# Kernel optimization log

Hardware: AMD Instinct MI355X
Metric: run time of the kernel (lower is better)

The kernel has to match this reference:

```python
import jax, jax.numpy as jnp
import numpy as np

NUM_CLASSES = 3
SMOOTH = 1e-5
EPS = 1e-6
ITERS = 8
W_CL = 0.5


def maxpool3d(x):
    # 3x3x3 max pool, stride 1, padding 1 (pads with -inf, matching torch max_pool3d)
    return jax.lax.reduce_window(
        x, -jnp.inf, jax.lax.max,
        window_dimensions=(1, 1, 3, 3, 3),
        window_strides=(1, 1, 1, 1, 1),
        padding=[(0, 0), (0, 0), (1, 1), (1, 1), (1, 1)])


def soft_skeletonize_3d(x, iters=ITERS):
    for _ in range(iters):
        eroded = 1.0 - maxpool3d(1.0 - x)
        opened = maxpool3d(eroded)
        contour = jax.nn.relu(opened - eroded)
        x = jax.nn.relu(x - contour)
    return x


def setup_inputs() -> dict:
    key = jax.random.key(0)
    k1, k2 = jax.random.split(key)
    logits = jax.random.normal(k1, (2, 3, 160, 160, 160), dtype=jnp.float32)
    target = jax.random.randint(k2, (2, 160, 160, 160), 0, NUM_CLASSES, dtype=jnp.int64)
    return {"logits": logits, "target": target}


def reference(logits, target):
    # ---- DiceCE ----
    logp = jax.nn.log_softmax(logits, axis=1)                      # [B,C,D,H,W]
    ce = -jnp.mean(jnp.take_along_axis(logp, target[:, None], axis=1))
    probs = jnp.exp(logp)
    onehot = jax.lax.stop_gradient(
        jax.nn.one_hot(target, NUM_CLASSES, axis=1, dtype=probs.dtype))
    dims = (0, 2, 3, 4)
    intersect = jnp.sum(probs * onehot, axis=dims)                 # [C]
    pred_sum = jnp.sum(probs, axis=dims)
    targ_sum = jnp.sum(onehot, axis=dims)
    dice_per_class = (2.0 * intersect + SMOOTH) / (pred_sum + targ_sum + SMOOTH)
    base = ce + (1.0 - jnp.mean(dice_per_class))
    # ---- soft clDice ----
    p_v = jnp.clip(1.0 - probs[:, :1], 0.0, 1.0)                   # [B,1,D,H,W]
    y_v = 1.0 - onehot[:, :1]
    p_skel = soft_skeletonize_3d(p_v)
    y_skel = soft_skeletonize_3d(y_v)
    tprec = jnp.sum(p_skel * y_v) / (jnp.sum(p_skel) + EPS)
    tsens = jnp.sum(y_skel * p_v) / (jnp.sum(y_skel) + EPS)
    cldice = 2.0 * tprec * tsens / (tprec + tsens + EPS)
    return base + W_CL * (1.0 - cldice)
```

## Files before the change

kernel.cpp:

```cpp
#include <hip/hip_runtime.h>
#include <math.h>

#define B_    2
#define DDIM  160
#define HDIM  160
#define WDIM  160
#define DHW   (DDIM*HDIM*WDIM)
#define NVOX  (B_*DHW)
#define NGRP  (NVOX/4)
#define ITERS 8
#define DT    4

#define SMOOTHF 1e-5
#define EPSF    1e-6
#define W_CL    0.5

#define NB1 2048
#define NQ1 10
#define NB2 2048
#define NQ2 4

#define NROWS (B_*DDIM*HDIM)
#define YW    8
#define NYW   (NROWS*YW)

#define P_THREADS (10*HDIM*(DDIM/DT)*B_)
#define P_BLOCKS  (P_THREADS/256)
#define Y_BLOCKS  (NROWS/256)
#define F_BLOCKS  (P_BLOCKS + Y_BLOCKS)

#define OFF_P1 0
#define OFF_P2 (NB1*NQ1*8)
#define HEADER_BYTES 262144


__device__ inline double wave_reduce(double v) {
    #pragma unroll
    for (int off = 32; off > 0; off >>= 1)
        v += __shfl_down(v, off, 64);
    return v;
}

template<int NQ>
__device__ inline void block_reduce_store(double* vals, double* out) {
    __shared__ double smem[NQ][4];
    int lane = threadIdx.x & 63;
    int wid  = threadIdx.x >> 6;
    #pragma unroll
    for (int q = 0; q < NQ; ++q) {
        double v = wave_reduce(vals[q]);
        if (lane == 0) smem[q][wid] = v;
    }
    __syncthreads();
    if (threadIdx.x == 0) {
        #pragma unroll
        for (int q = 0; q < NQ; ++q)
            out[q] = smem[q][0] + smem[q][1] + smem[q][2] + smem[q][3];
    }
}


__global__ void init_kernel(const float* __restrict__ logits,
                            const int*   __restrict__ target,
                            float* __restrict__ porig,
                            double* __restrict__ partials)
{
    double acc[NQ1];
    #pragma unroll
    for (int q = 0; q < NQ1; ++q) acc[q] = 0.0;

    int tid = blockIdx.x * blockDim.x + threadIdx.x;
    int stride = gridDim.x * blockDim.x;
    for (int g = tid; g < NGRP; g += stride) {
        int i = g * 4;
        int b = i / DHW;
        int s = i - b * DHW;
        const float* base = logits + (size_t)b * (3 * DHW) + s;
        float4 l0 = *(const float4*)(base);
        float4 l1 = *(const float4*)(base + DHW);
        float4 l2 = *(const float4*)(base + 2 * DHW);
        int4 tg = *(const int4*)(target + i);

        float pv[4];
        const float* a0 = (const float*)&l0;
        const float* a1 = (const float*)&l1;
        const float* a2 = (const float*)&l2;
        const int*   tt = (const int*)&tg;
        #pragma unroll
        for (int j = 0; j < 4; ++j) {
            float x0 = a0[j], x1 = a1[j], x2 = a2[j];
            float m  = fmaxf(x0, fmaxf(x1, x2));
            float e0 = __expf(x0 - m), e1 = __expf(x1 - m), e2 = __expf(x2 - m);
            float sum = e0 + e1 + e2;
            float inv = 1.0f / sum;
            float q0 = e0 * inv, q1 = e1 * inv, q2 = e2 * inv;
            int t = tt[j];
            float lt = (t == 0) ? x0 : ((t == 1) ? x1 : x2);
            float logp_t = (lt - m) - __logf(sum);
            acc[0] += (double)(-logp_t);
            acc[4] += (double)q0; acc[5] += (double)q1; acc[6] += (double)q2;
            if (t == 0)      { acc[1] += (double)q0; acc[7] += 1.0; }
            else if (t == 1) { acc[2] += (double)q1; acc[8] += 1.0; }
            else             { acc[3] += (double)q2; acc[9] += 1.0; }
            float p = 1.0f - q0;
            pv[j] = fminf(fmaxf(p, 0.0f), 1.0f);
        }
        *(float4*)(porig + i) = make_float4(pv[0], pv[1], pv[2], pv[3]);
    }
    block_reduce_store<NQ1>(acc, partials + (size_t)blockIdx.x * NQ1);
}


__global__ void ybits_init(const int* __restrict__ target,
                           unsigned* __restrict__ yb)
{
    int tid = blockIdx.x * 256 + threadIdx.x;
    int k = tid % YW;
    int rowlin = tid / YW;
    unsigned word = 0u;
    if (k < 5) {
        const int* t = target + (size_t)rowlin * WDIM + k * 32;
        #pragma unroll
        for (int q = 0; q < 8; ++q) {
            int4 v = *(const int4*)(t + q * 4);
            if (v.x) word |= 1u << (q * 4 + 0);
            if (v.y) word |= 1u << (q * 4 + 1);
            if (v.z) word |= 1u << (q * 4 + 2);
            if (v.w) word |= 1u << (q * 4 + 3);
        }
    }
    yb[tid] = word;
}


__device__ inline void row18(const float* __restrict__ row, int w0, float pad, float* e) {
    float4 f;
    f = *(const float4*)(row + 0);  e[1]=f.x;  e[2]=f.y;  e[3]=f.z;  e[4]=f.w;
    f = *(const float4*)(row + 4);  e[5]=f.x;  e[6]=f.y;  e[7]=f.z;  e[8]=f.w;
    f = *(const float4*)(row + 8);  e[9]=f.x;  e[10]=f.y; e[11]=f.z; e[12]=f.w;
    f = *(const float4*)(row + 12); e[13]=f.x; e[14]=f.y; e[15]=f.z; e[16]=f.w;
    e[0]  = (w0 > 0)         ? row[-1] : pad;
    e[17] = (w0 + 16 < WDIM) ? row[16] : pad;
}

__device__ inline void load_yrow(const unsigned* __restrict__ base, unsigned* r) {
    uint4 v = *(const uint4*)base;
    r[0] = v.x; r[1] = v.y; r[2] = v.z; r[3] = v.w; r[4] = base[4];
}

__device__ inline void werode_row(const unsigned* r, unsigned* out) {
    #pragma unroll
    for (int k = 0; k < 5; ++k) {
        unsigned l  = (r[k] << 1) | (k > 0 ? (r[k-1] >> 31) : 1u);
        unsigned rt = (r[k] >> 1) | (k < 4 ? (r[k+1] << 31) : 0x80000000u);
        out[k] = r[k] & l & rt;
    }
}

__device__ inline void wdilate_row(const unsigned* r, unsigned* out) {
    #pragma unroll
    for (int k = 0; k < 5; ++k) {
        unsigned l  = (r[k] << 1) | (k > 0 ? (r[k-1] >> 31) : 0u);
        unsigned rt = (r[k] >> 1) | (k < 4 ? (r[k+1] << 31) : 0u);
        out[k] = r[k] | l | rt;
    }
}


__global__ void fused_erode(const float* __restrict__ x, float* __restrict__ er,
                            const unsigned* __restrict__ yb, unsigned* __restrict__ eb)
{
    if (blockIdx.x < P_BLOCKS) {
        int tid = blockIdx.x * 256 + threadIdx.x;
        int w16 = tid % 10;
        int t2  = tid / 10;
        int h   = t2 % HDIM;
        int t3  = t2 / HDIM;
        int dc  = t3 % (DDIM / DT);
        int vol = t3 / (DDIM / DT);
        int w0  = w16 * 16;
        int d0  = dc * DT;
        const float* src = x + (size_t)vol * DHW;
        float*       dst = er + (size_t)vol * DHW;

        float ring[3][16];
        #pragma unroll
        for (int step = 0; step < DT + 2; ++step) {
            int d = d0 - 1 + step;
            float cur[16];
            #pragma unroll
            for (int i = 0; i < 16; ++i) cur[i] = INFINITY;
            if ((unsigned)d < (unsigned)DDIM) {
                #pragma unroll
                for (int dy = -1; dy <= 1; ++dy) {
                    int y = h + dy;
                    if ((unsigned)y >= (unsigned)HDIM) continue;
                    const float* row = src + ((size_t)d * HDIM + y) * WDIM + w0;
                    float e[18];
                    row18(row, w0, INFINITY, e);
                    #pragma unroll
                    for (int i = 0; i < 16; ++i)
                        cur[i] = fminf(cur[i], fminf(e[i], fminf(e[i+1], e[i+2])));
                }
            }
            #pragma unroll
            for (int i = 0; i < 16; ++i) ring[step % 3][i] = cur[i];
            if (step >= 2) {
                int dd = d - 1;
                float* o = dst + ((size_t)dd * HDIM + h) * WDIM + w0;
                #pragma unroll
                for (int q = 0; q < 4; ++q) {
                    float4 v;
                    v.x = fminf(ring[0][q*4+0], fminf(ring[1][q*4+0], ring[2][q*4+0]));
                    v.y = fminf(ring[0][q*4+1], fminf(ring[1][q*4+1], ring[2][q*4+1]));
                    v.z = fminf(ring[0][q*4+2], fminf(ring[1][q*4+2], ring[2][q*4+2]));
                    v.w = fminf(ring[0][q*4+3], fminf(ring[1][q*4+3], ring[2][q*4+3]));
                    *(float4*)(o + q*4) = v;
                }
            }
        }
    } else {
        int tid = (blockIdx.x - P_BLOCKS) * 256 + threadIdx.x;
        int h  = tid % HDIM;
        int t2 = tid / HDIM;
        int d  = t2 % DDIM;
        int b  = t2 / DDIM;
        unsigned acc[5] = {~0u, ~0u, ~0u, ~0u, ~0u};
        #pragma unroll
        for (int dz = -1; dz <= 1; ++dz) {
            int z = d + dz; if ((unsigned)z >= (unsigned)DDIM) continue;
            #pragma unroll
            for (int dy = -1; dy <= 1; ++dy) {
                int y = h + dy; if ((unsigned)y >= (unsigned)HDIM) continue;
                unsigned r[5], we[5];
                load_yrow(yb + ((size_t)(b * DDIM + z) * HDIM + y) * YW, r);
                werode_row(r, we);
                #pragma unroll
                for (int k = 0; k < 5; ++k) acc[k] &= we[k];
            }
        }
        unsigned* o = eb + (size_t)tid * YW;
        *(uint4*)o = make_uint4(acc[0], acc[1], acc[2], acc[3]);
        o[4] = acc[4];
    }
}


__global__ void fused_open(const float* __restrict__ er,
                           const float* __restrict__ xsrc, float* __restrict__ xdst,
                           const unsigned* __restrict__ eb, unsigned* __restrict__ yb)
{
    if (blockIdx.x < P_BLOCKS) {
        int tid = blockIdx.x * 256 + threadIdx.x;
        int w16 = tid % 10;
        int t2  = tid / 10;
        int h   = t2 % HDIM;
        int t3  = t2 / HDIM;
        int dc  = t3 % (DDIM / DT);
        int vol = t3 / (DDIM / DT);
        int w0  = w16 * 16;
        int d0  = dc * DT;
        const float* ers = er + (size_t)vol * DHW;
        const float* xs  = xsrc + (size_t)vol * DHW;
        float*       xb  = xdst + (size_t)vol * DHW;

        float ring[3][16];
        #pragma unroll
        for (int step = 0; step < DT + 2; ++step) {
            int d = d0 - 1 + step;
            float cur[16];
            #pragma unroll
            for (int i = 0; i < 16; ++i) cur[i] = -INFINITY;
            if ((unsigned)d < (unsigned)DDIM) {
                #pragma unroll
                for (int dy = -1; dy <= 1; ++dy) {
                    int y = h + dy;
                    if ((unsigned)y >= (unsigned)HDIM) continue;
                    const float* row = ers + ((size_t)d * HDIM + y) * WDIM + w0;
                    float e[18];
                    row18(row, w0, -INFINITY, e);
                    #pragma unroll
                    for (int i = 0; i < 16; ++i)
                        cur[i] = fmaxf(cur[i], fmaxf(e[i], fmaxf(e[i+1], e[i+2])));
                }
            }
            #pragma unroll
            for (int i = 0; i < 16; ++i) ring[step % 3][i] = cur[i];
            if (step >= 2) {
                int dd = d - 1;
                size_t idx = ((size_t)dd * HDIM + h) * WDIM + w0;
                #pragma unroll
                for (int q = 0; q < 4; ++q) {
                    float4 ec = *(const float4*)(ers + idx + q*4);
                    float4 xv = *(const float4*)(xs + idx + q*4);
                    float o0 = fmaxf(ring[0][q*4+0], fmaxf(ring[1][q*4+0], ring[2][q*4+0]));
                    float o1 = fmaxf(ring[0][q*4+1], fmaxf(ring[1][q*4+1], ring[2][q*4+1]));
                    float o2 = fmaxf(ring[0][q*4+2], fmaxf(ring[1][q*4+2], ring[2][q*4+2]));
                    float o3 = fmaxf(ring[0][q*4+3], fmaxf(ring[1][q*4+3], ring[2][q*4+3]));
                    float4 r;
                    r.x = fmaxf(xv.x - fmaxf(o0 - ec.x, 0.0f), 0.0f);
                    r.y = fmaxf(xv.y - fmaxf(o1 - ec.y, 0.0f), 0.0f);
                    r.z = fmaxf(xv.z - fmaxf(o2 - ec.z, 0.0f), 0.0f);
                    r.w = fmaxf(xv.w - fmaxf(o3 - ec.w, 0.0f), 0.0f);
                    *(float4*)(xb + idx + q*4) = r;
                }
            }
        }
    } else {
        int tid = (blockIdx.x - P_BLOCKS) * 256 + threadIdx.x;
        int h  = tid % HDIM;
        int t2 = tid / HDIM;
        int d  = t2 % DDIM;
        int b  = t2 / DDIM;
        unsigned acc[5] = {0u, 0u, 0u, 0u, 0u};
        unsigned ecen[5];
        #pragma unroll
        for (int dz = -1; dz <= 1; ++dz) {
            int z = d + dz; if ((unsigned)z >= (unsigned)DDIM) continue;
            #pragma unroll
            for (int dy = -1; dy <= 1; ++dy) {
                int y = h + dy; if ((unsigned)y >= (unsigned)HDIM) continue;
                unsigned r[5], wd[5];
                load_yrow(eb + ((size_t)(b * DDIM + z) * HDIM + y) * YW, r);
                if (dz == 0 && dy == 0) {
                    #pragma unroll
                    for (int k = 0; k < 5; ++k) ecen[k] = r[k];
                }
                wdilate_row(r, wd);
                #pragma unroll
                for (int k = 0; k < 5; ++k) acc[k] |= wd[k];
            }
        }
        unsigned* yo = yb + (size_t)tid * YW;
        unsigned yr[5];
        load_yrow(yo, yr);
        unsigned out[5];
        #pragma unroll
        for (int k = 0; k < 5; ++k)
            out[k] = yr[k] & ~(acc[k] & ~ecen[k]);
        *(uint4*)yo = make_uint4(out[0], out[1], out[2], out[3]);
        yo[4] = out[4];
    }
}


__global__ void final_reduce_kernel(const float* __restrict__ porig,
                                    const float* __restrict__ pskel,
                                    const int*   __restrict__ target,
                                    const unsigned* __restrict__ yb,
                                    double* __restrict__ partials)
{
    double acc[NQ2];
    #pragma unroll
    for (int q = 0; q < NQ2; ++q) acc[q] = 0.0;

    int tid = blockIdx.x * blockDim.x + threadIdx.x;
    int stride = gridDim.x * blockDim.x;
    for (int g = tid; g < NGRP; g += stride) {
        int i = g * 4;
        float4 ps = *(const float4*)(pskel + i);
        float4 po = *(const float4*)(porig + i);
        int4   tg = *(const int4*)(target + i);
        int w = i % WDIM;
        int rowlin = i / WDIM;
        unsigned word = yb[(size_t)rowlin * YW + (w >> 5)];
        unsigned b4 = (word >> (w & 31)) & 0xFu;
        const float* psp = (const float*)&ps;
        const float* pop = (const float*)&po;
        const int*   tp  = (const int*)&tg;
        #pragma unroll
        for (int j = 0; j < 4; ++j) {
            float yv  = (tp[j] != 0) ? 1.0f : 0.0f;
            float ysk = (float)((b4 >> j) & 1u);
            acc[0] += (double)(psp[j] * yv);
            acc[1] += (double)psp[j];
            acc[2] += (double)(ysk * pop[j]);
            acc[3] += (double)ysk;
        }
    }
    block_reduce_store<NQ2>(acc, partials + (size_t)blockIdx.x * NQ2);
}


__global__ void finalize_kernel(const double* __restrict__ p1,
                                const double* __restrict__ p2,
                                float* __restrict__ out)
{
    double acc[NQ1 + NQ2];
    #pragma unroll
    for (int q = 0; q < NQ1 + NQ2; ++q) acc[q] = 0.0;

    for (int b = threadIdx.x; b < NB1; b += 256) {
        #pragma unroll
        for (int q = 0; q < NQ1; ++q) acc[q] += p1[(size_t)b * NQ1 + q];
    }
    for (int b = threadIdx.x; b < NB2; b += 256) {
        #pragma unroll
        for (int q = 0; q < NQ2; ++q) acc[NQ1 + q] += p2[(size_t)b * NQ2 + q];
    }

    __shared__ double smem[NQ1 + NQ2][4];
    int lane = threadIdx.x & 63;
    int wid  = threadIdx.x >> 6;
    #pragma unroll
    for (int q = 0; q < NQ1 + NQ2; ++q) {
        double v = wave_reduce(acc[q]);
        if (lane == 0) smem[q][wid] = v;
    }
    __syncthreads();
    if (threadIdx.x == 0) {
        double a[NQ1 + NQ2];
        #pragma unroll
        for (int q = 0; q < NQ1 + NQ2; ++q)
            a[q] = smem[q][0] + smem[q][1] + smem[q][2] + smem[q][3];

        double ce = a[0] / (double)NVOX;
        double dice = 0.0;
        #pragma unroll
        for (int c = 0; c < 3; ++c) {
            double I = a[1 + c], P = a[4 + c], T = a[7 + c];
            dice += (2.0 * I + SMOOTHF) / (P + T + SMOOTHF);
        }
        dice *= (1.0 / 3.0);
        double base = ce + (1.0 - dice);

        double tprec = a[10] / (a[11] + EPSF);
        double tsens = a[12] / (a[13] + EPSF);
        double cld = 2.0 * tprec * tsens / (tprec + tsens + EPSF);
        out[0] = (float)(base + W_CL * (1.0 - cld));
    }
}


extern "C" void kernel_launch(void* const* d_in, const int* in_sizes, int n_in,
                              void* d_out, int out_size, void* d_ws, size_t ws_size,
                              hipStream_t stream) {
    const float* logits = (const float*)d_in[0];
    const int*   target = (const int*)d_in[1];

    double* partials1 = (double*)((char*)d_ws + OFF_P1);
    double* partials2 = (double*)((char*)d_ws + OFF_P2);
    float*  porig = (float*)((char*)d_ws + HEADER_BYTES);
    float*  pskel = porig + NVOX;
    float*  er    = pskel + NVOX;
    unsigned* ybits  = (unsigned*)(er + NVOX);
    unsigned* yebits = ybits + NYW;

    init_kernel<<<NB1, 256, 0, stream>>>(logits, target, porig, partials1);
    ybits_init<<<NYW / 256, 256, 0, stream>>>(target, ybits);

    for (int it = 0; it < ITERS; ++it) {
        const float* xsrc = (it == 0) ? porig : pskel;
        fused_erode<<<F_BLOCKS, 256, 0, stream>>>(xsrc, er, ybits, yebits);
        fused_open<<<F_BLOCKS, 256, 0, stream>>>(er, xsrc, pskel, yebits, ybits);
    }

    final_reduce_kernel<<<NB2, 256, 0, stream>>>(porig, pskel, target, ybits, partials2);
    finalize_kernel<<<1, 256, 0, stream>>>(partials1, partials2, (float*)d_out);
}
```

Measured before the change: 656.3 us.

## Store skeleton field in fp16 and do min/max on raw half bits

```diff
diff --git a/kernel.cpp b/kernel.cpp
--- a/kernel.cpp
+++ b/kernel.cpp
@@ -1,4 +1,5 @@
 #include <hip/hip_runtime.h>
+#include <hip/hip_fp16.h>
 #include <math.h>
 
 #define B_    2
@@ -29,9 +30,25 @@
 #define Y_BLOCKS  (NROWS/256)
 #define F_BLOCKS  (P_BLOCKS + Y_BLOCKS)
 
+#define PAD_MIN 0x7C00u
+#define PAD_MAX 0x0000u
+
 #define OFF_P1 0
 #define OFF_P2 (NB1*NQ1*8)
 #define HEADER_BYTES 262144
+
+typedef unsigned short u16;
+
+
+__device__ inline u16 umn(u16 a, u16 b) { return a < b ? a : b; }
+__device__ inline u16 umx(u16 a, u16 b) { return a > b ? a : b; }
+
+__device__ inline float us2f(u16 u) {
+    __half h; __builtin_memcpy(&h, &u, 2); return __half2float(h);
+}
+__device__ inline u16 f2us(float f) {
+    __half h = __float2half(f); u16 u; __builtin_memcpy(&u, &h, 2); return u;
+}
 
 
 __device__ inline double wave_reduce(double v) {
@@ -63,11 +80,12 @@
 __global__ void init_kernel(const float* __restrict__ logits,
                             const int*   __restrict__ target,
                             float* __restrict__ porig,
+                            u16*   __restrict__ p16,
                             double* __restrict__ partials)
 {
-    double acc[NQ1];
-    #pragma unroll
-    for (int q = 0; q < NQ1; ++q) acc[q] = 0.0;
+    float facc[NQ1];
+    #pragma unroll
+    for (int q = 0; q < NQ1; ++q) facc[q] = 0.0f;
 
     int tid = blockIdx.x * blockDim.x + threadIdx.x;
     int stride = gridDim.x * blockDim.x;
@@ -97,16 +115,23 @@
             int t = tt[j];
             float lt = (t == 0) ? x0 : ((t == 1) ? x1 : x2);
             float logp_t = (lt - m) - __logf(sum);
-            acc[0] += (double)(-logp_t);
-            acc[4] += (double)q0; acc[5] += (double)q1; acc[6] += (double)q2;
-            if (t == 0)      { acc[1] += (double)q0; acc[7] += 1.0; }
-            else if (t == 1) { acc[2] += (double)q1; acc[8] += 1.0; }
-            else             { acc[3] += (double)q2; acc[9] += 1.0; }
+            facc[0] += -logp_t;
+            facc[4] += q0; facc[5] += q1; facc[6] += q2;
+            if (t == 0)      { facc[1] += q0; facc[7] += 1.0f; }
+            else if (t == 1) { facc[2] += q1; facc[8] += 1.0f; }
+            else             { facc[3] += q2; facc[9] += 1.0f; }
             float p = 1.0f - q0;
             pv[j] = fminf(fmaxf(p, 0.0f), 1.0f);
         }
         *(float4*)(porig + i) = make_float4(pv[0], pv[1], pv[2], pv[3]);
-    }
+        union { uint2 v; u16 u[4]; } ph;
+        #pragma unroll
+        for (int j = 0; j < 4; ++j) ph.u[j] = f2us(pv[j]);
+        *(uint2*)(p16 + i) = ph.v;
+    }
+    double acc[NQ1];
+    #pragma unroll
+    for (int q = 0; q < NQ1; ++q) acc[q] = (double)facc[q];
     block_reduce_store<NQ1>(acc, partials + (size_t)blockIdx.x * NQ1);
 }
 
@@ -133,14 +158,22 @@
 }
 
 
-__device__ inline void row18(const float* __restrict__ row, int w0, float pad, float* e) {
-    float4 f;
-    f = *(const float4*)(row + 0);  e[1]=f.x;  e[2]=f.y;  e[3]=f.z;  e[4]=f.w;
-    f = *(const float4*)(row + 4);  e[5]=f.x;  e[6]=f.y;  e[7]=f.z;  e[8]=f.w;
-    f = *(const float4*)(row + 8);  e[9]=f.x;  e[10]=f.y; e[11]=f.z; e[12]=f.w;
-    f = *(const float4*)(row + 12); e[13]=f.x; e[14]=f.y; e[15]=f.z; e[16]=f.w;
+__device__ inline void rowload_h(const u16* __restrict__ row, int w0, u16 pad, u16* e) {
+    union { uint4 v; u16 u[8]; } a, b;
+    a.v = *(const uint4*)(row);
+    b.v = *(const uint4*)(row + 8);
+    #pragma unroll
+    for (int i = 0; i < 8; ++i) { e[1 + i] = a.u[i]; e[9 + i] = b.u[i]; }
     e[0]  = (w0 > 0)         ? row[-1] : pad;
     e[17] = (w0 + 16 < WDIM) ? row[16] : pad;
+}
+
+__device__ inline void store16_h(u16* __restrict__ o, const u16* v) {
+    union { uint4 q; u16 u[8]; } s0, s1;
+    #pragma unroll
+    for (int i = 0; i < 8; ++i) { s0.u[i] = v[i]; s1.u[i] = v[8 + i]; }
+    *(uint4*)(o)     = s0.q;
+    *(uint4*)(o + 8) = s1.q;
 }
 
 __device__ inline void load_yrow(const unsigned* __restrict__ base, unsigned* r) {
@@ -167,7 +200,7 @@
 }
 
 
-__global__ void fused_erode(const float* __restrict__ x, float* __restrict__ er,
+__global__ void fused_erode(const u16* __restrict__ x, u16* __restrict__ er,
                             const unsigned* __restrict__ yb, unsigned* __restrict__ eb)
 {
     if (blockIdx.x < P_BLOCKS) {
@@ -180,43 +213,38 @@
         int vol = t3 / (DDIM / DT);
         int w0  = w16 * 16;
         int d0  = dc * DT;
-        const float* src = x + (size_t)vol * DHW;
-        float*       dst = er + (size_t)vol * DHW;
-
-        float ring[3][16];
+        const u16* src = x + (size_t)vol * DHW;
+        u16*       dst = er + (size_t)vol * DHW;
+
+        u16 ring[3][16];
         #pragma unroll
         for (int step = 0; step < DT + 2; ++step) {
             int d = d0 - 1 + step;
-            float cur[16];
-            #pragma unroll
-            for (int i = 0; i < 16; ++i) cur[i] = INFINITY;
+            u16 cur[16];
+            #pragma unroll
+            for (int i = 0; i < 16; ++i) cur[i] = PAD_MIN;
             if ((unsigned)d < (unsigned)DDIM) {
                 #pragma unroll
                 for (int dy = -1; dy <= 1; ++dy) {
                     int y = h + dy;
                     if ((unsigned)y >= (unsigned)HDIM) continue;
-                    const float* row = src + ((size_t)d * HDIM + y) * WDIM + w0;
-                    float e[18];
-                    row18(row, w0, INFINITY, e);
+                    const u16* row = src + ((size_t)d * HDIM + y) * WDIM + w0;
+                    u16 e[18];
+                    rowload_h(row, w0, PAD_MIN, e);
                     #pragma unroll
                     for (int i = 0; i < 16; ++i)
-                        cur[i] = fminf(cur[i], fminf(e[i], fminf(e[i+1], e[i+2])));
+                        cur[i] = umn(cur[i], umn(e[i], umn(e[i+1], e[i+2])));
                 }
             }
             #pragma unroll
             for (int i = 0; i < 16; ++i) ring[step % 3][i] = cur[i];
             if (step >= 2) {
                 int dd = d - 1;
-                float* o = dst + ((size_t)dd * HDIM + h) * WDIM + w0;
-                #pragma unroll
-                for (int q = 0; q < 4; ++q) {
-                    float4 v;
-                    v.x = fminf(ring[0][q*4+0], fminf(ring[1][q*4+0], ring[2][q*4+0]));
-                    v.y = fminf(ring[0][q*4+1], fminf(ring[1][q*4+1], ring[2][q*4+1]));
-                    v.z = fminf(ring[0][q*4+2], fminf(ring[1][q*4+2], ring[2][q*4+2]));
-                    v.w = fminf(ring[0][q*4+3], fminf(ring[1][q*4+3], ring[2][q*4+3]));
-                    *(float4*)(o + q*4) = v;
-                }
+                u16 out[16];
+                #pragma unroll
+                for (int i = 0; i < 16; ++i)
+                    out[i] = umn(ring[0][i], umn(ring[1][i], ring[2][i]));
+                store16_h(dst + ((size_t)dd * HDIM + h) * WDIM + w0, out);
             }
         }
     } else {
@@ -246,8 +274,8 @@
 }
 
 
-__global__ void fused_open(const float* __restrict__ er,
-                           const float* __restrict__ xsrc, float* __restrict__ xdst,
+__global__ void fused_open(const u16* __restrict__ er,
+                           const u16* __restrict__ xsrc, u16* __restrict__ xdst,
                            const unsigned* __restrict__ eb, unsigned* __restrict__ yb)
 {
     if (blockIdx.x < P_BLOCKS) {
@@ -260,28 +288,28 @@
         int vol = t3 / (DDIM / DT);
         int w0  = w16 * 16;
         int d0  = dc * DT;
-        const float* ers = er + (size_t)vol * DHW;
-        const float* xs  = xsrc + (size_t)vol * DHW;
-        float*       xb  = xdst + (size_t)vol * DHW;
-
-        float ring[3][16];
+        const u16* ers = er + (size_t)vol * DHW;
+        const u16* xs  = xsrc + (size_t)vol * DHW;
+        u16*       xb  = xdst + (size_t)vol * DHW;
+
+        u16 ring[3][16];
         #pragma unroll
         for (int step = 0; step < DT + 2; ++step) {
             int d = d0 - 1 + step;
-            float cur[16];
-            #pragma unroll
-            for (int i = 0; i < 16; ++i) cur[i] = -INFINITY;
+            u16 cur[16];
+            #pragma unroll
+            for (int i = 0; i < 16; ++i) cur[i] = PAD_MAX;
             if ((unsigned)d < (unsigned)DDIM) {
                 #pragma unroll
                 for (int dy = -1; dy <= 1; ++dy) {
                     int y = h + dy;
                     if ((unsigned)y >= (unsigned)HDIM) continue;
-                    const float* row = ers + ((size_t)d * HDIM + y) * WDIM + w0;
-                    float e[18];
-                    row18(row, w0, -INFINITY, e);
+                    const u16* row = ers + ((size_t)d * HDIM + y) * WDIM + w0;
+                    u16 e[18];
+                    rowload_h(row, w0, PAD_MAX, e);
                     #pragma unroll
                     for (int i = 0; i < 16; ++i)
-                        cur[i] = fmaxf(cur[i], fmaxf(e[i], fmaxf(e[i+1], e[i+2])));
+                        cur[i] = umx(cur[i], umx(e[i], umx(e[i+1], e[i+2])));
                 }
             }
             #pragma unroll
@@ -289,21 +317,20 @@
             if (step >= 2) {
                 int dd = d - 1;
                 size_t idx = ((size_t)dd * HDIM + h) * WDIM + w0;
-                #pragma unroll
-                for (int q = 0; q < 4; ++q) {
-                    float4 ec = *(const float4*)(ers + idx + q*4);
-                    float4 xv = *(const float4*)(xs + idx + q*4);
-                    float o0 = fmaxf(ring[0][q*4+0], fmaxf(ring[1][q*4+0], ring[2][q*4+0]));
-                    float o1 = fmaxf(ring[0][q*4+1], fmaxf(ring[1][q*4+1], ring[2][q*4+1]));
-                    float o2 = fmaxf(ring[0][q*4+2], fmaxf(ring[1][q*4+2], ring[2][q*4+2]));
-                    float o3 = fmaxf(ring[0][q*4+3], fmaxf(ring[1][q*4+3], ring[2][q*4+3]));
-                    float4 r;
-                    r.x = fmaxf(xv.x - fmaxf(o0 - ec.x, 0.0f), 0.0f);
-                    r.y = fmaxf(xv.y - fmaxf(o1 - ec.y, 0.0f), 0.0f);
-                    r.z = fmaxf(xv.z - fmaxf(o2 - ec.z, 0.0f), 0.0f);
-                    r.w = fmaxf(xv.w - fmaxf(o3 - ec.w, 0.0f), 0.0f);
-                    *(float4*)(xb + idx + q*4) = r;
+                union { uint4 v; u16 u[8]; } ec0, ec1, xv0, xv1;
+                ec0.v = *(const uint4*)(ers + idx);
+                ec1.v = *(const uint4*)(ers + idx + 8);
+                xv0.v = *(const uint4*)(xs + idx);
+                xv1.v = *(const uint4*)(xs + idx + 8);
+                u16 out[16];
+                #pragma unroll
+                for (int i = 0; i < 16; ++i) {
+                    float of = us2f(umx(ring[0][i], umx(ring[1][i], ring[2][i])));
+                    float ef = us2f(i < 8 ? ec0.u[i] : ec1.u[i - 8]);
+                    float xf = us2f(i < 8 ? xv0.u[i] : xv1.u[i - 8]);
+                    out[i] = f2us(fmaxf(xf - fmaxf(of - ef, 0.0f), 0.0f));
                 }
+                store16_h(xb + idx, out);
             }
         }
     } else {
@@ -345,7 +372,7 @@
 
 
 __global__ void final_reduce_kernel(const float* __restrict__ porig,
-                                    const float* __restrict__ pskel,
+                                    const u16*   __restrict__ pskel,
                                     const int*   __restrict__ target,
                                     const unsigned* __restrict__ yb,
                                     double* __restrict__ partials)
@@ -358,22 +385,23 @@
     int stride = gridDim.x * blockDim.x;
     for (int g = tid; g < NGRP; g += stride) {
         int i = g * 4;
-        float4 ps = *(const float4*)(pskel + i);
+        union { uint2 v; u16 u[4]; } ps;
+        ps.v = *(const uint2*)(pskel + i);
         float4 po = *(const float4*)(porig + i);
         int4   tg = *(const int4*)(target + i);
         int w = i % WDIM;
         int rowlin = i / WDIM;
         unsigned word = yb[(size_t)rowlin * YW + (w >> 5)];
         unsigned b4 = (word >> (w & 31)) & 0xFu;
-        const float* psp = (const float*)&ps;
         const float* pop = (const float*)&po;
         const int*   tp  = (const int*)&tg;
         #pragma unroll
         for (int j = 0; j < 4; ++j) {
+            float psf = us2f(ps.u[j]);
             float yv  = (tp[j] != 0) ? 1.0f : 0.0f;
             float ysk = (float)((b4 >> j) & 1u);
-            acc[0] += (double)(psp[j] * yv);
-            acc[1] += (double)psp[j];
+            acc[0] += (double)(psf * yv);
+            acc[1] += (double)psf;
             acc[2] += (double)(ysk * pop[j]);
             acc[3] += (double)ysk;
         }
@@ -441,20 +469,23 @@
     double* partials1 = (double*)((char*)d_ws + OFF_P1);
     double* partials2 = (double*)((char*)d_ws + OFF_P2);
     float*  porig = (float*)((char*)d_ws + HEADER_BYTES);
-    float*  pskel = porig + NVOX;
-    float*  er    = pskel + NVOX;
-    unsigned* ybits  = (unsigned*)(er + NVOX);
-    unsigned* yebits = ybits + NYW;
-
-    init_kernel<<<NB1, 256, 0, stream>>>(logits, target, porig, partials1);
-    ybits_init<<<NYW / 256, 256, 0, stream>>>(target, ybits);
-
+    u16*    pA    = (u16*)(porig + NVOX);
+    u16*    pB    = pA + NVOX;
+    u16*    erH   = pB + NVOX;
+    unsigned* yb0 = (unsigned*)(erH + NVOX);
+    unsigned* yb1 = yb0 + NYW;
+
+    init_kernel<<<NB1, 256, 0, stream>>>(logits, target, porig, pA, partials1);
+    ybits_init<<<NYW / 256, 256, 0, stream>>>(target, yb0);
+
+    u16* cur = pA;
+    u16* nxt = pB;
     for (int it = 0; it < ITERS; ++it) {
-        const float* xsrc = (it == 0) ? porig : pskel;
-        fused_erode<<<F_BLOCKS, 256, 0, stream>>>(xsrc, er, ybits, yebits);
-        fused_open<<<F_BLOCKS, 256, 0, stream>>>(er, xsrc, pskel, yebits, ybits);
-    }
-
-    final_reduce_kernel<<<NB2, 256, 0, stream>>>(porig, pskel, target, ybits, partials2);
+        fused_erode<<<F_BLOCKS, 256, 0, stream>>>(cur, erH, yb0, yb1);
+        fused_open<<<F_BLOCKS, 256, 0, stream>>>(erH, cur, nxt, yb1, yb0);
+        u16* t = cur; cur = nxt; nxt = t;
+    }
+
+    final_reduce_kernel<<<NB2, 256, 0, stream>>>(porig, cur, target, yb0, partials2);
     finalize_kernel<<<1, 256, 0, stream>>>(partials1, partials2, (float*)d_out);
 }
```

Result: faster. 618.1 us (-5.8%).
